# Kernel tuning notes

Hardware: AMD Instinct MI355X
Metric: run time of the kernel (lower is better)

## Reference

```python
import jax, jax.numpy as jnp
import numpy as np


def setup_inputs() -> dict:
    key = jax.random.key(0)
    k1, k2 = jax.random.split(key)
    N, D, E = 16384, 4096, 64  # tokens, n_embd, n_exp
    x = jax.random.normal(k1, (N, D), dtype=jnp.float32)
    W = jax.random.normal(k2, (E, D), dtype=jnp.float32) * 0.02  # w_gate weight [n_exp, n_embd]
    return {"x": x, "W": W, "top_k": 4, "n_groups": 8, "n_limited_groups": 4}


def reference(x, W, top_k, n_groups, n_limited_groups):
    ROUTE_SCALE = 1.0
    N = x.shape[0]
    E = W.shape[0]
    exp_per_group = E // n_groups

    logits = x @ W.T                      # [N, E] gate linear (bias=False)
    scores = jax.nn.softmax(logits, -1)   # func == 'softmax'

    # group-limited routing: pick top n_limited_groups groups by max score (bias=False path)
    gs = scores.reshape(N, n_groups, exp_per_group)
    group_scores = gs.max(axis=-1)                             # [N, G]
    _, top_grp = jax.lax.top_k(group_scores, n_limited_groups)  # [N, L]
    selected = jnp.any(
        jnp.arange(n_groups)[None, None, :] == top_grp[:, :, None], axis=1
    )                                                           # [N, G] bool
    masked = jnp.where(selected[:, :, None], gs, -jnp.inf).reshape(N, E)

    # top-k experts over unmasked scores; weights are the gathered scores
    topk_vals, topk_idx = jax.lax.top_k(masked, top_k)          # [N, K]
    weights = (topk_vals * ROUTE_SCALE).astype(x.dtype)         # softmax -> no renorm

    # histc over expert ids
    counts = jnp.zeros((E,), jnp.int32).at[topk_idx.reshape(-1)].add(1)
    return weights, topk_idx, counts
```

## Files before the change

### kernel.cpp

```cpp
#include <hip/hip_runtime.h>
#include <math.h>

#define NTOK 16384
#define DDIM 4096
#define NEXP 64
#define KTOP 4

#define SPLITK 8
#define KPER (DDIM / SPLITK)
#define BK 32
#define NCH (KPER / BK)
#define BMB 256

typedef __attribute__((ext_vector_type(8))) short short8;
typedef __attribute__((ext_vector_type(4))) float f32x4;


__device__ __forceinline__ unsigned short f2bf_rtn(float x) {
    unsigned int b = __float_as_uint(x);
    return (unsigned short)((b + 0x7FFFu + ((b >> 16) & 1u)) >> 16);
}
__device__ __forceinline__ float bf2f(unsigned short h) {
    return __uint_as_float(((unsigned int)h) << 16);
}

__global__ __launch_bounds__(256) void prep_kernel(
    const float* __restrict__ W, unsigned short* __restrict__ Whi,
    unsigned short* __restrict__ Wlo, float* __restrict__ counts)
{
    int idx = blockIdx.x * 256 + threadIdx.x;
    float x = W[idx];
    unsigned short h = f2bf_rtn(x);
    float lo = x - bf2f(h);
    Whi[idx] = h;
    Wlo[idx] = f2bf_rtn(lo);
    if (blockIdx.x == 0 && threadIdx.x < NEXP) counts[threadIdx.x] = 0.0f;
}

__global__ __launch_bounds__(512, 2) void gemm_kernel(
    const float* __restrict__ X, const unsigned short* __restrict__ Whi,
    const unsigned short* __restrict__ Wlo, float* __restrict__ part)
{
    __shared__ unsigned short sHi[NEXP * KPER];
    __shared__ unsigned short sLo[NEXP * KPER];

    const int tid  = threadIdx.x;
    const int lane = tid & 63;
    const int w    = tid >> 6;
    const int tb   = blockIdx.x >> 3;
    const int s    = blockIdx.x & 7;
    const int kbase = s * KPER;
    const int tok0 = tb * BMB + w * 32;

    {
        const int e = tid >> 3;
        const int j = tid & 7;
        const unsigned short* gh = Whi + (size_t)e * DDIM + kbase + j * 8;
        const unsigned short* gl = Wlo + (size_t)e * DDIM + kbase + j * 8;
        const int m = (e & 7) * 8;
        #pragma unroll
        for (int i = 0; i < 8; ++i) {
            const int kk = j * 8 + i * 64;
            short8 vh = *(const short8*)(gh + i * 64);
            short8 vl = *(const short8*)(gl + i * 64);
            *(short8*)&sHi[e * KPER + (kk ^ m)] = vh;
            *(short8*)&sLo[e * KPER + (kk ^ m)] = vl;
        }
    }
    __syncthreads();

    const int fr = lane & 15;
    const int fg = lane >> 4;
    const int kx = (fg * 8) ^ ((fr & 7) * 8);

    const float* __restrict__ xa0 = X + (size_t)(tok0 + fr) * DDIM + kbase + fg * 8;
    const float* __restrict__ xa1 = xa0 + (size_t)16 * DDIM;

    f32x4 acc[2][4];
    #pragma unroll
    for (int mg = 0; mg < 2; ++mg)
        #pragma unroll
        for (int ng = 0; ng < 4; ++ng)
            acc[mg][ng] = (f32x4){0.f, 0.f, 0.f, 0.f};

    float4 xq[NCH][2][2];

#define LOADA(c)                                                            \
    {                                                                       \
        xq[c][0][0] = *(const float4*)(xa0 + (c) * BK);                     \
        xq[c][0][1] = *(const float4*)(xa0 + (c) * BK + 4);                 \
        xq[c][1][0] = *(const float4*)(xa1 + (c) * BK);                     \
        xq[c][1][1] = *(const float4*)(xa1 + (c) * BK + 4);                 \
    }

    LOADA(0)
    LOADA(1)

    #pragma unroll
    for (int c = 0; c < NCH; ++c) {
        if (c + 2 < NCH) LOADA(c + 2)

        short8 ahi[2], alo[2];
        #pragma unroll
        for (int mg = 0; mg < 2; ++mg) {
            #pragma unroll
            for (int j = 0; j < 8; ++j) {
                const float4 q = xq[c][mg][j >> 2];
                float xv = ((j & 3) == 0) ? q.x : ((j & 3) == 1) ? q.y
                         : ((j & 3) == 2) ? q.z : q.w;
                unsigned short h = f2bf_rtn(xv);
                float lo = xv - bf2f(h);
                ahi[mg][j] = (short)h;
                alo[mg][j] = (short)(__float_as_uint(lo) >> 16);
            }
        }

        #pragma unroll
        for (int ng = 0; ng < 4; ++ng) {
            const int bE = (ng * 16 + fr) * KPER;
            const int t  = (c * BK) ^ kx;
            const short8 bh = *(const short8*)(sHi + bE + t);
            const short8 bl = *(const short8*)(sLo + bE + t);
            #pragma unroll
            for (int mg = 0; mg < 2; ++mg) {
                acc[mg][ng] = __builtin_amdgcn_mfma_f32_16x16x32_bf16(
                    ahi[mg], bh, acc[mg][ng], 0, 0, 0);
                acc[mg][ng] = __builtin_amdgcn_mfma_f32_16x16x32_bf16(
                    ahi[mg], bl, acc[mg][ng], 0, 0, 0);
                acc[mg][ng] = __builtin_amdgcn_mfma_f32_16x16x32_bf16(
                    alo[mg], bh, acc[mg][ng], 0, 0, 0);
            }
        }
    }
#undef LOADA

    #pragma unroll
    for (int mg = 0; mg < 2; ++mg)
        #pragma unroll
        for (int r = 0; r < 4; ++r) {
            const int row = tok0 + mg * 16 + fg * 4 + r;
            float* __restrict__ pp = part + ((size_t)row * SPLITK + s) * NEXP;
            #pragma unroll
            for (int ng = 0; ng < 4; ++ng)
                pp[ng * 16 + fr] = acc[mg][ng][r];
        }
}

__global__ __launch_bounds__(256) void route_kernel(
    const float* __restrict__ part, float* __restrict__ outW,
    float* __restrict__ outI, float* __restrict__ counts)
{
    __shared__ int hist[NEXP];
    const int tid = threadIdx.x;
    if (tid < NEXP) hist[tid] = 0;
    __syncthreads();

    const int lane = tid & 63;
    const int wv   = tid >> 6;
    const int tok_base = blockIdx.x * 32 + wv * 8;

    for (int t = 0; t < 8; ++t) {
        const int n = tok_base + t;
        float L = 0.0f;
        #pragma unroll
        for (int s = 0; s < SPLITK; ++s)
            L += part[((size_t)n * SPLITK + s) * NEXP + lane];

        float m = L;
        #pragma unroll
        for (int off = 32; off > 0; off >>= 1) m = fmaxf(m, __shfl_xor(m, off));
        float p = expf(L - m);
        float ssum = p;
        #pragma unroll
        for (int off = 32; off > 0; off >>= 1) ssum += __shfl_xor(ssum, off);
        float score = p / ssum;

        float gm = score;
        gm = fmaxf(gm, __shfl_xor(gm, 1));
        gm = fmaxf(gm, __shfl_xor(gm, 2));
        gm = fmaxf(gm, __shfl_xor(gm, 4));

        float ga[8];
        #pragma unroll
        for (int g = 0; g < 8; ++g) ga[g] = __shfl(gm, g * 8);
        unsigned selmask = 0u;
        #pragma unroll
        for (int r = 0; r < 4; ++r) {
            float best = -INFINITY; int bg = 0;
            #pragma unroll
            for (int g = 0; g < 8; ++g) {
                bool taken  = (selmask >> g) & 1u;
                bool better = (!taken) && (ga[g] > best);
                bg   = better ? g : bg;
                best = better ? ga[g] : best;
            }
            selmask |= (1u << bg);
        }

        float ms = ((selmask >> (lane >> 3)) & 1u) ? score : -INFINITY;
        float wk[4]; int wi[4];
        #pragma unroll
        for (int r = 0; r < 4; ++r) {
            float v = ms; int ix = lane;
            #pragma unroll
            for (int off = 32; off > 0; off >>= 1) {
                float vo = __shfl_xor(v, off);
                int   io = __shfl_xor(ix, off);
                if (vo > v || (vo == v && io < ix)) { v = vo; ix = io; }
            }
            wk[r] = v; wi[r] = ix;
            if (lane == ix) ms = -INFINITY;
        }

        if (lane == 0) {
            *(float4*)&outW[(size_t)n * 4] = make_float4(wk[0], wk[1], wk[2], wk[3]);
            *(float4*)&outI[(size_t)n * 4] =
                make_float4((float)wi[0], (float)wi[1], (float)wi[2], (float)wi[3]);
            atomicAdd(&hist[wi[0]], 1);
            atomicAdd(&hist[wi[1]], 1);
            atomicAdd(&hist[wi[2]], 1);
            atomicAdd(&hist[wi[3]], 1);
        }
    }

    __syncthreads();
    if (tid < NEXP) atomicAdd(&counts[tid], (float)hist[tid]);
}

extern "C" void kernel_launch(void* const* d_in, const int* in_sizes, int n_in,
                              void* d_out, int out_size, void* d_ws, size_t ws_size,
                              hipStream_t stream) {
    const float* X = (const float*)d_in[0];
    const float* W = (const float*)d_in[1];

    float* outW   = (float*)d_out;
    float* outI   = outW + (size_t)NTOK * KTOP;
    float* counts = outW + (size_t)2 * NTOK * KTOP;

    float*          part = (float*)d_ws;
    unsigned short* Whi  = (unsigned short*)(part + (size_t)NTOK * SPLITK * NEXP);
    unsigned short* Wlo  = Whi + (size_t)NEXP * DDIM;

    prep_kernel<<<(NEXP * DDIM) / 256, 256, 0, stream>>>(W, Whi, Wlo, counts);
    gemm_kernel<<<(NTOK / BMB) * SPLITK, 512, 0, stream>>>(X, Whi, Wlo, part);
    route_kernel<<<NTOK / 32, 256, 0, stream>>>(part, outW, outI, counts);
}
```

Measured before the change: 105.4 us.

## Stream X and W tiles through double-buffered LDS with direct global-to-LDS loads

The GEMM no longer stages the whole W slice in LDS and no longer loads X straight into registers. Each stage now copies swizzled X and Whi/Wlo tiles into double-buffered LDS with global_load_lds, prefetches the next stage while computing, and syncs once per stage. This shrinks LDS use enough to raise the occupancy hint to 4 blocks per CU. The X hi/lo split now truncates with bit masks instead of round-to-nearest, which cuts ALU work but changes the rounding of the hi/lo pair.

```diff
diff --git a/kernel.cpp b/kernel.cpp
--- a/kernel.cpp
+++ b/kernel.cpp
@@ -9,7 +9,7 @@
 #define SPLITK 8
 #define KPER (DDIM / SPLITK)
 #define BK 32
-#define NCH (KPER / BK)
+#define NSTG (KPER / BK)
 #define BMB 256
 
 typedef __attribute__((ext_vector_type(8))) short short8;
@@ -22,6 +22,17 @@
 }
 __device__ __forceinline__ float bf2f(unsigned short h) {
     return __uint_as_float(((unsigned int)h) << 16);
+}
+__device__ __forceinline__ short8 mk8(unsigned int a, unsigned int b,
+                                      unsigned int c, unsigned int d) {
+    union { unsigned int u[4]; short8 s; } p;
+    p.u[0] = a; p.u[1] = b; p.u[2] = c; p.u[3] = d;
+    return p.s;
+}
+__device__ __forceinline__ void gl2lds16(const void* g, void* l) {
+    __builtin_amdgcn_global_load_lds(
+        (const __attribute__((address_space(1))) unsigned int*)g,
+        (__attribute__((address_space(3))) unsigned int*)l, 16, 0, 0);
 }
 
 __global__ __launch_bounds__(256) void prep_kernel(
@@ -37,12 +48,13 @@
     if (blockIdx.x == 0 && threadIdx.x < NEXP) counts[threadIdx.x] = 0.0f;
 }
 
-__global__ __launch_bounds__(512, 2) void gemm_kernel(
+__global__ __launch_bounds__(512, 4) void gemm_kernel(
     const float* __restrict__ X, const unsigned short* __restrict__ Whi,
     const unsigned short* __restrict__ Wlo, float* __restrict__ part)
 {
-    __shared__ unsigned short sHi[NEXP * KPER];
-    __shared__ unsigned short sLo[NEXP * KPER];
+    __shared__ float          sX[2][BMB * BK];
+    __shared__ unsigned short sH[2][NEXP * BK];
+    __shared__ unsigned short sL[2][NEXP * BK];
 
     const int tid  = threadIdx.x;
     const int lane = tid & 63;
@@ -50,31 +62,40 @@
     const int tb   = blockIdx.x >> 3;
     const int s    = blockIdx.x & 7;
     const int kbase = s * KPER;
-    const int tok0 = tb * BMB + w * 32;
-
-    {
-        const int e = tid >> 3;
-        const int j = tid & 7;
-        const unsigned short* gh = Whi + (size_t)e * DDIM + kbase + j * 8;
-        const unsigned short* gl = Wlo + (size_t)e * DDIM + kbase + j * 8;
-        const int m = (e & 7) * 8;
-        #pragma unroll
-        for (int i = 0; i < 8; ++i) {
-            const int kk = j * 8 + i * 64;
-            short8 vh = *(const short8*)(gh + i * 64);
-            short8 vl = *(const short8*)(gl + i * 64);
-            *(short8*)&sHi[e * KPER + (kk ^ m)] = vh;
-            *(short8*)&sLo[e * KPER + (kk ^ m)] = vl;
-        }
+    const int tok0 = tb * BMB;
+
+    const float* xsrc[4];
+    int xdst[4];
+    #pragma unroll
+    for (int i = 0; i < 4; ++i) {
+        const int seg = i * 8 + w;
+        const int o   = seg * 256 + lane * 4;
+        const int row = o >> 5;
+        const int cp  = o & 31;
+        const int sw  = ((row & 4) << 1) | ((row & 8) >> 1);
+        xsrc[i] = X + (size_t)(tok0 + row) * DDIM + kbase + (cp ^ sw);
+        xdst[i] = seg * 256;
     }
+    const int wseg = w & 3;
+    const int wo   = wseg * 512 + lane * 8;
+    const int we   = wo >> 5;
+    const int wkk  = wo & 31;
+    const unsigned short* wsrc =
+        ((w < 4) ? Whi : Wlo) + (size_t)we * DDIM + kbase + (wkk ^ ((we & 3) * 8));
+
+    #pragma unroll
+    for (int i = 0; i < 4; ++i) gl2lds16(xsrc[i], &sX[0][xdst[i]]);
+    gl2lds16(wsrc, (w < 4) ? (void*)&sH[0][wseg * 512] : (void*)&sL[0][wseg * 512]);
     __syncthreads();
 
     const int fr = lane & 15;
     const int fg = lane >> 4;
-    const int kx = (fg * 8) ^ ((fr & 7) * 8);
-
-    const float* __restrict__ xa0 = X + (size_t)(tok0 + fr) * DDIM + kbase + fg * 8;
-    const float* __restrict__ xa1 = xa0 + (size_t)16 * DDIM;
+    const int sw  = ((fr & 4) << 1) | ((fr & 8) >> 1);
+    const int fo0 = (fg * 8) ^ sw;
+    const int fo1 = (fg * 8 + 4) ^ sw;
+    const int frow0 = (w * 32 + fr) * BK;
+    const int frow1 = frow0 + 16 * BK;
+    const int bt  = (fg * 8) ^ ((fr & 3) * 8);
 
     f32x4 acc[2][4];
     #pragma unroll
@@ -83,44 +104,61 @@
         for (int ng = 0; ng < 4; ++ng)
             acc[mg][ng] = (f32x4){0.f, 0.f, 0.f, 0.f};
 
-    float4 xq[NCH][2][2];
-
-#define LOADA(c)                                                            \
-    {                                                                       \
-        xq[c][0][0] = *(const float4*)(xa0 + (c) * BK);                     \
-        xq[c][0][1] = *(const float4*)(xa0 + (c) * BK + 4);                 \
-        xq[c][1][0] = *(const float4*)(xa1 + (c) * BK);                     \
-        xq[c][1][1] = *(const float4*)(xa1 + (c) * BK + 4);                 \
-    }
-
-    LOADA(0)
-    LOADA(1)
-
-    #pragma unroll
-    for (int c = 0; c < NCH; ++c) {
-        if (c + 2 < NCH) LOADA(c + 2)
+    for (int st = 0; st < NSTG; ++st) {
+        const float*          cx = sX[st & 1];
+        const unsigned short* ch = sH[st & 1];
+        const unsigned short* cl = sL[st & 1];
+
+        if (st + 1 < NSTG) {
+            const int nb = (st + 1) & 1;
+            #pragma unroll
+            for (int i = 0; i < 4; ++i)
+                gl2lds16(xsrc[i] + (st + 1) * BK, &sX[nb][xdst[i]]);
+            gl2lds16(wsrc + (st + 1) * BK,
+                     (w < 4) ? (void*)&sH[nb][wseg * 512]
+                             : (void*)&sL[nb][wseg * 512]);
+        }
+
+        const float4 a00 = *(const float4*)&cx[frow0 + fo0];
+        const float4 a01 = *(const float4*)&cx[frow0 + fo1];
+        const float4 a10 = *(const float4*)&cx[frow1 + fo0];
+        const float4 a11 = *(const float4*)&cx[frow1 + fo1];
 
         short8 ahi[2], alo[2];
         #pragma unroll
         for (int mg = 0; mg < 2; ++mg) {
-            #pragma unroll
-            for (int j = 0; j < 8; ++j) {
-                const float4 q = xq[c][mg][j >> 2];
-                float xv = ((j & 3) == 0) ? q.x : ((j & 3) == 1) ? q.y
-                         : ((j & 3) == 2) ? q.z : q.w;
-                unsigned short h = f2bf_rtn(xv);
-                float lo = xv - bf2f(h);
-                ahi[mg][j] = (short)h;
-                alo[mg][j] = (short)(__float_as_uint(lo) >> 16);
-            }
+            const float4 qa = mg ? a10 : a00;
+            const float4 qb = mg ? a11 : a01;
+            unsigned int hi[4], lo[4];
+            const unsigned int u0 = __float_as_uint(qa.x), u1 = __float_as_uint(qa.y);
+            const unsigned int u2 = __float_as_uint(qa.z), u3 = __float_as_uint(qa.w);
+            const unsigned int u4 = __float_as_uint(qb.x), u5 = __float_as_uint(qb.y);
+            const unsigned int u6 = __float_as_uint(qb.z), u7 = __float_as_uint(qb.w);
+            hi[0] = (u0 >> 16) | (u1 & 0xFFFF0000u);
+            hi[1] = (u2 >> 16) | (u3 & 0xFFFF0000u);
+            hi[2] = (u4 >> 16) | (u5 & 0xFFFF0000u);
+            hi[3] = (u6 >> 16) | (u7 & 0xFFFF0000u);
+            const float l0 = qa.x - __uint_as_float(u0 & 0xFFFF0000u);
+            const float l1 = qa.y - __uint_as_float(u1 & 0xFFFF0000u);
+            const float l2 = qa.z - __uint_as_float(u2 & 0xFFFF0000u);
+            const float l3 = qa.w - __uint_as_float(u3 & 0xFFFF0000u);
+            const float l4 = qb.x - __uint_as_float(u4 & 0xFFFF0000u);
+            const float l5 = qb.y - __uint_as_float(u5 & 0xFFFF0000u);
+            const float l6 = qb.z - __uint_as_float(u6 & 0xFFFF0000u);
+            const float l7 = qb.w - __uint_as_float(u7 & 0xFFFF0000u);
+            lo[0] = (__float_as_uint(l0) >> 16) | (__float_as_uint(l1) & 0xFFFF0000u);
+            lo[1] = (__float_as_uint(l2) >> 16) | (__float_as_uint(l3) & 0xFFFF0000u);
+            lo[2] = (__float_as_uint(l4) >> 16) | (__float_as_uint(l5) & 0xFFFF0000u);
+            lo[3] = (__float_as_uint(l6) >> 16) | (__float_as_uint(l7) & 0xFFFF0000u);
+            ahi[mg] = mk8(hi[0], hi[1], hi[2], hi[3]);
+            alo[mg] = mk8(lo[0], lo[1], lo[2], lo[3]);
         }
 
         #pragma unroll
         for (int ng = 0; ng < 4; ++ng) {
-            const int bE = (ng * 16 + fr) * KPER;
-            const int t  = (c * BK) ^ kx;
-            const short8 bh = *(const short8*)(sHi + bE + t);
-            const short8 bl = *(const short8*)(sLo + bE + t);
+            const int bo = (ng * 16 + fr) * BK + bt;
+            const short8 bh = *(const short8*)&ch[bo];
+            const short8 bl = *(const short8*)&cl[bo];
             #pragma unroll
             for (int mg = 0; mg < 2; ++mg) {
                 acc[mg][ng] = __builtin_amdgcn_mfma_f32_16x16x32_bf16(
@@ -131,14 +169,15 @@
                     alo[mg], bh, acc[mg][ng], 0, 0, 0);
             }
         }
+
+        __syncthreads();
     }
-#undef LOADA
 
     #pragma unroll
     for (int mg = 0; mg < 2; ++mg)
         #pragma unroll
         for (int r = 0; r < 4; ++r) {
-            const int row = tok0 + mg * 16 + fg * 4 + r;
+            const int row = tok0 + w * 32 + mg * 16 + fg * 4 + r;
             float* __restrict__ pp = part + ((size_t)row * SPLITK + s) * NEXP;
             #pragma unroll
             for (int ng = 0; ng < 4; ++ng)
```

New measurement: 101.3 us. -3.9%, faster.
